# Kernel tuning notes

Measured on AMD Instinct MI355X. Metric: run time of the kernel, lower is better.

The kernel has to match this reference:

```python
import jax, jax.numpy as jnp
import numpy as np

NPOINT = 2048
NSAMPLE = 16
LEAKY = 0.1
BN_EPS = 1e-5


def square_distance(src, dst):
    # src [B,S,3], dst [B,N,3] -> [B,S,N] squared euclidean
    d = -2.0 * jnp.einsum('bsc,bnc->bsn', src, dst)
    d = d + jnp.sum(src * src, -1)[:, :, None]
    d = d + jnp.sum(dst * dst, -1)[:, None, :]
    return d


def furthest_point_sample(xyz, npoint):
    # xyz [B,N,3] -> idx [B,npoint]; matches pointnet2 CUDA (seed = index 0)
    B, N, _ = xyz.shape

    def step(carry, _):
        dist, far = carry  # dist [B,N], far [B]
        centroid = jnp.take_along_axis(xyz, far[:, None, None], axis=1)  # [B,1,3]
        d = jnp.sum((xyz - centroid) ** 2, axis=-1)
        dist = jnp.minimum(dist, d)
        nxt = jnp.argmax(dist, axis=-1).astype(jnp.int32)
        return (dist, nxt), far

    init = (jnp.full((B, N), 1e10, xyz.dtype), jnp.zeros((B,), jnp.int32))
    _, idxs = jax.lax.scan(step, init, None, length=npoint)
    return idxs.T  # [B, npoint]


def _gather_nbrs(p, i):
    # p [N,C], i [S,K] -> [S,K,C]
    return p[i]


gather_group = jax.vmap(_gather_nbrs)


def conv_bn_lrelu(x, W, g, b):
    # x [B,Cin,S,K], W [Cout,Cin]; 1x1 conv + train-mode BatchNorm2d + LeakyReLU
    y = jnp.einsum('oc,bcsk->bosk', W, x)
    mean = jnp.mean(y, axis=(0, 2, 3), keepdims=True)
    var = jnp.var(y, axis=(0, 2, 3), keepdims=True)
    y = (y - mean) * jax.lax.rsqrt(var + BN_EPS)
    y = y * g[None, :, None, None] + b[None, :, None, None]
    return jnp.where(y > 0, y, LEAKY * y)


def setup_inputs() -> dict:
    key = jax.random.key(0)
    ks = jax.random.split(key, 5)
    B, N, D = 4, 8192, 64
    return {
        'xyz': jax.random.normal(ks[0], (B, 3, N), jnp.float32),
        'points': jax.random.normal(ks[1], (B, D, N), jnp.float32),
        'conv0_w': jax.random.normal(ks[2], (64, 67), jnp.float32) * 0.05,
        'conv1_w': jax.random.normal(ks[3], (64, 64), jnp.float32) * 0.05,
        'conv2_w': jax.random.normal(ks[4], (128, 64), jnp.float32) * 0.05,
        'bn0_g': jnp.ones((64,), jnp.float32),
        'bn0_b': jnp.zeros((64,), jnp.float32),
        'bn1_g': jnp.ones((64,), jnp.float32),
        'bn1_b': jnp.zeros((64,), jnp.float32),
        'bn2_g': jnp.ones((128,), jnp.float32),
        'bn2_b': jnp.zeros((128,), jnp.float32),
    }


def reference(xyz, points, conv0_w, conv1_w, conv2_w,
              bn0_g, bn0_b, bn1_g, bn1_b, bn2_g, bn2_b):
    xyz_t = jnp.transpose(xyz, (0, 2, 1))      # [B,N,3]
    pts_t = jnp.transpose(points, (0, 2, 1))   # [B,N,D]

    fps_idx = furthest_point_sample(xyz_t, NPOINT)                       # [B,S]
    new_xyz = jnp.take_along_axis(xyz_t, fps_idx[:, :, None], axis=1)    # [B,S,3]

    sqrd = square_distance(new_xyz, xyz_t)                               # [B,S,N]
    _, idx = jax.lax.top_k(-sqrd, NSAMPLE)                               # [B,S,K]

    grouped_xyz = gather_group(xyz_t, idx)                               # [B,S,K,3]
    grouped_norm = grouped_xyz - new_xyz[:, :, None, :]
    grouped_pts = gather_group(pts_t, idx)                               # [B,S,K,D]
    new_points = jnp.concatenate([grouped_norm, grouped_pts], axis=-1)   # [B,S,K,D+3]
    new_points = jnp.transpose(new_points, (0, 3, 1, 2))                 # [B,D+3,S,K]

    for W, g, b in ((conv0_w, bn0_g, bn0_b), (conv1_w, bn1_g, bn1_b),
                    (conv2_w, bn2_g, bn2_b)):
        new_points = conv_bn_lrelu(new_points, W, g, b)

    feat = jnp.max(new_points, axis=-1)                                  # [B,128,S]
    return jnp.transpose(new_xyz, (0, 2, 1)), feat, fps_idx
```

## Files before the change

### kernel.cpp

```cpp
#include <hip/hip_runtime.h>
#include <hip/hip_bf16.h>

#define BB 4
#define NP 8192
#define SS 2048
#define KK 16
#define DD 64
#define NN (BB*SS*KK)
#define HEATERS 128

typedef float vf2 __attribute__((ext_vector_type(2)));

#if defined(__has_builtin)
#if __has_builtin(__builtin_amdgcn_permlane16_swap) && __has_builtin(__builtin_amdgcn_permlane32_swap)
#define HAVE_PERMLANE_SWAP 1
#endif
#endif

__device__ __forceinline__ float wave_max_f32(float v) {
  int x;
  x = __builtin_amdgcn_update_dpp(0, __float_as_int(v), 0xB1, 0xF, 0xF, true);
  v = fmaxf(v, __int_as_float(x));
  x = __builtin_amdgcn_update_dpp(0, __float_as_int(v), 0x4E, 0xF, 0xF, true);
  v = fmaxf(v, __int_as_float(x));
  x = __builtin_amdgcn_update_dpp(0, __float_as_int(v), 0x141, 0xF, 0xF, true);
  v = fmaxf(v, __int_as_float(x));
  x = __builtin_amdgcn_update_dpp(0, __float_as_int(v), 0x140, 0xF, 0xF, true);
  v = fmaxf(v, __int_as_float(x));
#ifdef HAVE_PERMLANE_SWAP
  {
    unsigned u = __float_as_uint(v);
    auto r16 = __builtin_amdgcn_permlane16_swap(u, u, false, false);
    v = fmaxf(__uint_as_float(r16[0]), __uint_as_float(r16[1]));
    unsigned u2 = __float_as_uint(v);
    auto r32 = __builtin_amdgcn_permlane32_swap(u2, u2, false, false);
    v = fmaxf(__uint_as_float(r32[0]), __uint_as_float(r32[1]));
  }
#else
  x = __builtin_amdgcn_ds_swizzle(__float_as_int(v), 0x401F);
  v = fmaxf(v, __int_as_float(x));
  v = fmaxf(v, __shfl_xor(v, 32, 64));
#endif
  return v;
}

__global__ __launch_bounds__(512) void fps_kernel(
    const float* __restrict__ xyz, float* __restrict__ newXyz,
    float* __restrict__ out, int* __restrict__ done)
{
  const int t = threadIdx.x;

  if (blockIdx.x >= BB) {
    float a0 = 1.0f, a1 = 1.1f, a2 = 1.2f, a3 = 1.3f;
    const float bm = 1.000001f, cm = 1e-7f;
    for (;;) {
      for (int k = 0; k < 1024; k++) {
        a0 = __builtin_fmaf(a0, bm, cm);
        a1 = __builtin_fmaf(a1, bm, cm);
        a2 = __builtin_fmaf(a2, bm, cm);
        a3 = __builtin_fmaf(a3, bm, cm);
      }
      if (__hip_atomic_load(done, __ATOMIC_RELAXED, __HIP_MEMORY_SCOPE_AGENT) >= BB)
        break;
    }
    if (a0 == 123.456f && a1 == 2.f && a2 == 3.f && a3 == 4.f)
      ((volatile int*)done)[1] = 1;
    return;
  }

  const int b = blockIdx.x;
  const float* xb = xyz + (size_t)b * 3 * NP;

  __shared__ float lx[NP], ly[NP], lz[NP];
  __shared__ int   wis[SS];
  __shared__ unsigned long long swin[3];

  vf2 px[8], py[8], pz[8], dist[8];
  const int i0 = t << 4;
#pragma unroll
  for (int h = 0; h < 8; h++) {
    int i = i0 + (h << 1);
    vf2 x = *(const vf2*)(xb + i);
    vf2 y = *(const vf2*)(xb + NP + i);
    vf2 z = *(const vf2*)(xb + 2 * NP + i);
    px[h] = x; py[h] = y; pz[h] = z;
    dist[h] = (vf2){1e10f, 1e10f};
    *(vf2*)(lx + i) = x; *(vf2*)(ly + i) = y; *(vf2*)(lz + i) = z;
  }
  if (t == 0) { wis[0] = 0; swin[0] = 0; swin[1] = 0; swin[2] = 0; }
  __syncthreads();

  float cx = lx[0], cy = ly[0], cz = lz[0];

  for (int it = 1; it < SS; ++it) {
    vf2 c2x = {cx, cx}, c2y = {cy, cy}, c2z = {cz, cz};
    vf2 lb = {-1.0f, -1.0f};
    {
#pragma clang fp contract(off)
#pragma unroll
      for (int h = 0; h < 8; h++) {
        vf2 dx = px[h] - c2x;
        vf2 dy = py[h] - c2y;
        vf2 dz = pz[h] - c2z;
        vf2 d  = (dx * dx + dy * dy) + dz * dz;
        vf2 dm = __builtin_elementwise_min(dist[h], d);
        dist[h] = dm;
        lb = __builtin_elementwise_max(lb, dm);
      }
    }
    float lbest = fmaxf(lb.x, lb.y);
    float Vw = wave_max_f32(lbest);
    int q = it % 3;
    if (lbest == Vw) {
      unsigned mi = 0u;
#pragma unroll
      for (int h = 7; h >= 0; h--) {
        unsigned base = (unsigned)(i0 + (h << 1));
        if (dist[h].y == Vw) mi = base + 1;
        if (dist[h].x == Vw) mi = base;
      }
      unsigned long long pk =
          ((unsigned long long)__float_as_uint(Vw) << 32) | (unsigned)(~mi);
      atomicMax(&swin[q], pk);
    }
    __syncthreads();
    unsigned long long pkf = swin[q];
    int ii = (int)(~((unsigned)pkf));
    if (t == 0) { wis[it] = ii; swin[(q + 2) % 3] = 0; }
    cx = lx[ii]; cy = ly[ii]; cz = lz[ii];
  }
  __syncthreads();

  float* outX = out;
  float* outI = out + 24576 + 1048576;
  for (int s = t; s < SS; s += 512) {
    int iw = wis[s];
    float x = lx[iw], y = ly[iw], z = lz[iw];
    size_t qq = (size_t)(b * SS + s);
    newXyz[qq * 3 + 0] = x;
    newXyz[qq * 3 + 1] = y;
    newXyz[qq * 3 + 2] = z;
    outX[(b * 3 + 0) * SS + s] = x;
    outX[(b * 3 + 1) * SS + s] = y;
    outX[(b * 3 + 2) * SS + s] = z;
    outI[b * SS + s] = (float)iw;
  }
  if (t == 0)
    __hip_atomic_fetch_add(done, 1, __ATOMIC_RELEASE, __HIP_MEMORY_SCOPE_AGENT);
}

__global__ __launch_bounds__(256) void knn_kernel(
    const float* __restrict__ xyz, const float* __restrict__ newXyz,
    int* __restrict__ knnIdx)
{
  const int t = threadIdx.x, w = t >> 6, l = t & 63;
  const int q = blockIdx.x * 4 + w;
  const int b = q >> 11;
  const float* xb = xyz + (size_t)b * 3 * NP;
  float qx = newXyz[q * 3], qy = newXyz[q * 3 + 1], qz = newXyz[q * 3 + 2];
  float ss = __fadd_rn(__fadd_rn(__fmul_rn(qx, qx), __fmul_rn(qy, qy)), __fmul_rn(qz, qz));
  float kd[16]; int ki[16];
#pragma unroll
  for (int j = 0; j < 16; j++) { kd[j] = __builtin_inff(); ki[j] = 0x7fffffff; }

  for (int m = 0; m < 128; m++) {
    int i = l + (m << 6);
    float x = xb[i], y = xb[NP + i], z = xb[2 * NP + i];
    float dot = __fadd_rn(__fadd_rn(__fmul_rn(x, qx), __fmul_rn(y, qy)), __fmul_rn(z, qz));
    float nn  = __fadd_rn(__fadd_rn(__fmul_rn(x, x), __fmul_rn(y, y)), __fmul_rn(z, z));
    float d   = __fadd_rn(__fadd_rn(__fmul_rn(-2.0f, dot), ss), nn);
    if (d < kd[15]) {
      kd[15] = d; ki[15] = i;
#pragma unroll
      for (int jj = 15; jj >= 1; jj--) {
        if (kd[jj] < kd[jj - 1]) {
          float td = kd[jj]; kd[jj] = kd[jj - 1]; kd[jj - 1] = td;
          int   ti = ki[jj]; ki[jj] = ki[jj - 1]; ki[jj - 1] = ti;
        }
      }
    }
  }

  __shared__ float sd[4 * 64 * 17];
  __shared__ int   sx[4 * 64 * 17];
  int base = (w * 64 + l) * 17;
#pragma unroll
  for (int j = 0; j < 16; j++) { sd[base + j] = kd[j]; sx[base + j] = ki[j]; }
  __syncthreads();

  int cur = 0; int outIdx = 0;
#pragma unroll 1
  for (int r = 0; r < 16; r++) {
    float hv = (cur < 16) ? sd[base + cur] : __builtin_inff();
    int   hi = (cur < 16) ? sx[base + cur] : 0x7fffffff;
    int   hl = l;
#pragma unroll
    for (int m2 = 1; m2 < 64; m2 <<= 1) {
      float ov = __shfl_xor(hv, m2, 64);
      int   oi = __shfl_xor(hi, m2, 64);
      int   ol = __shfl_xor(hl, m2, 64);
      if (ov < hv || (ov == hv && oi < hi)) { hv = ov; hi = oi; hl = ol; }
    }
    if (l == hl) cur++;
    if (l == r) outIdx = hi;
  }
  if (l < 16) knnIdx[q * 16 + l] = outIdx;
}

__global__ __launch_bounds__(256) void build_x0(
    const float* __restrict__ xyz, const float* __restrict__ points,
    const float* __restrict__ newXyz, const int* __restrict__ knnIdx,
    float* __restrict__ X)
{
  int n = blockIdx.x * 256 + threadIdx.x;
  int b = n >> 15;
  int q = n >> 4;
  int ip = knnIdx[n];
  const float* xb = xyz + (size_t)b * 3 * NP;
  X[(size_t)0 * NN + n] = xb[ip]          - newXyz[q * 3 + 0];
  X[(size_t)1 * NN + n] = xb[NP + ip]     - newXyz[q * 3 + 1];
  X[(size_t)2 * NN + n] = xb[2 * NP + ip] - newXyz[q * 3 + 2];
  const float* pb = points + (size_t)b * DD * NP;
#pragma unroll 8
  for (int d0 = 0; d0 < DD; d0++)
    X[(size_t)(3 + d0) * NN + n] = pb[(size_t)d0 * NP + ip];
}

template <int CIN, int COUT, bool BNIN>
__global__ __launch_bounds__(256) void conv_kernel(
    const float* __restrict__ X, const float* __restrict__ W,
    const float* __restrict__ ss, float* __restrict__ Y)
{
  __shared__ vf2 sss[CIN];
  if (BNIN) {
    for (int i = threadIdx.x; i < CIN; i += 256) sss[i] = ((const vf2*)ss)[i];
    __syncthreads();
  }
  int n = blockIdx.x * 256 + threadIdx.x;
  float x[CIN];
#pragma unroll
  for (int c = 0; c < CIN; c++) x[c] = X[(size_t)c * NN + n];
  if (BNIN) {
#pragma unroll
    for (int c = 0; c < CIN; c++) {
      vf2 p = sss[c];
      float v = fmaf(x[c], p.x, p.y);
      x[c] = v > 0.0f ? v : 0.1f * v;
    }
  }
#pragma unroll 1
  for (int o = 0; o < COUT; o += 4) {
    float a0 = 0.f, a1 = 0.f, a2 = 0.f, a3 = 0.f;
#pragma unroll
    for (int c = 0; c < CIN; c++) {
      float xv = x[c];
      a0 = fmaf(W[(o + 0) * CIN + c], xv, a0);
      a1 = fmaf(W[(o + 1) * CIN + c], xv, a1);
      a2 = fmaf(W[(o + 2) * CIN + c], xv, a2);
      a3 = fmaf(W[(o + 3) * CIN + c], xv, a3);
    }
    Y[(size_t)(o + 0) * NN + n] = a0;
    Y[(size_t)(o + 1) * NN + n] = a1;
    Y[(size_t)(o + 2) * NN + n] = a2;
    Y[(size_t)(o + 3) * NN + n] = a3;
  }
}

__global__ __launch_bounds__(256) void stats_kernel(
    const float* __restrict__ Y, float* __restrict__ stats)
{
  int c = blockIdx.y;
  int base = blockIdx.x * 4096 + threadIdx.x;
  const float* yc = Y + (size_t)c * NN;
  float s1 = 0.f, s2 = 0.f;
#pragma unroll
  for (int j = 0; j < 16; j++) {
    float v = yc[base + j * 256];
    s1 += v; s2 = fmaf(v, v, s2);
  }
#pragma unroll
  for (int m = 1; m < 64; m <<= 1) {
    s1 += __shfl_xor(s1, m, 64);
    s2 += __shfl_xor(s2, m, 64);
  }
  __shared__ float r1[4], r2[4];
  int w = threadIdx.x >> 6;
  if ((threadIdx.x & 63) == 0) { r1[w] = s1; r2[w] = s2; }
  __syncthreads();
  if (threadIdx.x == 0) {
    float t1 = r1[0] + r1[1] + r1[2] + r1[3];
    float t2 = r2[0] + r2[1] + r2[2] + r2[3];
    atomicAdd(&stats[c * 2], t1);
    atomicAdd(&stats[c * 2 + 1], t2);
  }
}

template <int C>
__global__ void finalize_kernel(const float* __restrict__ stats,
                                const float* __restrict__ g,
                                const float* __restrict__ bt,
                                float* __restrict__ ss)
{
  int c = threadIdx.x;
  if (c < C) {
    float mean = stats[c * 2] * (1.0f / NN);
    float var  = stats[c * 2 + 1] * (1.0f / NN) - mean * mean;
    float inv  = rsqrtf(var + 1e-5f);
    float sc = inv * g[c];
    float sh = bt[c] - mean * sc;
    ss[c * 2] = sc; ss[c * 2 + 1] = sh;
  }
}

__global__ __launch_bounds__(256) void maxk_kernel(
    const float* __restrict__ X, const float* __restrict__ ss,
    float* __restrict__ out)
{
  int m = blockIdx.x * 256 + threadIdx.x;
  int s = m & 2047;
  int o = (m >> 11) & 127;
  int b = m >> 18;
  float sc = ss[2 * o], sh = ss[2 * o + 1];
  const float4* p = (const float4*)(X + (size_t)o * NN + ((size_t)((b << 11) + s) << 4));
  float mx = -__builtin_inff();
#pragma unroll
  for (int j = 0; j < 4; j++) {
    float4 v4 = p[j];
    float a = fmaf(v4.x, sc, sh); a = a > 0.f ? a : 0.1f * a;
    float b2 = fmaf(v4.y, sc, sh); b2 = b2 > 0.f ? b2 : 0.1f * b2;
    float c = fmaf(v4.z, sc, sh); c = c > 0.f ? c : 0.1f * c;
    float d = fmaf(v4.w, sc, sh); d = d > 0.f ? d : 0.1f * d;
    mx = fmaxf(mx, fmaxf(fmaxf(a, b2), fmaxf(c, d)));
  }
  out[24576 + (size_t)((b << 7) + o) * SS + s] = mx;
}

extern "C" void kernel_launch(void* const* d_in, const int* in_sizes, int n_in,
                              void* d_out, int out_size, void* d_ws, size_t ws_size,
                              hipStream_t stream) {
  const float* xyz    = (const float*)d_in[0];
  const float* points = (const float*)d_in[1];
  const float* w0 = (const float*)d_in[2];
  const float* w1 = (const float*)d_in[3];
  const float* w2 = (const float*)d_in[4];
  const float* g0 = (const float*)d_in[5];
  const float* b0 = (const float*)d_in[6];
  const float* g1 = (const float*)d_in[7];
  const float* b1 = (const float*)d_in[8];
  const float* g2 = (const float*)d_in[9];
  const float* b2 = (const float*)d_in[10];
  float* out = (float*)d_out;

  float* wsf    = (float*)d_ws;
  float* newXyz = wsf;
  int*   knnIdx = (int*)(wsf + 24576);
  float* stats0 = wsf + 155648;
  float* stats1 = wsf + 155904;
  float* stats2 = wsf + 156160;
  float* ss0    = wsf + 156416;
  float* ss1    = wsf + 156672;
  float* ss2    = wsf + 156928;
  int*   done   = (int*)(wsf + 157440);
  float* Xa     = wsf + 160000;
  float* Xb     = wsf + 8941824;

  hipMemsetAsync(stats0, 0, 2048 * 4, stream);

  fps_kernel<<<BB + HEATERS, 512, 0, stream>>>(xyz, newXyz, out, done);
  knn_kernel<<<SS * BB / 4, 256, 0, stream>>>(xyz, newXyz, knnIdx);
  build_x0<<<NN / 256, 256, 0, stream>>>(xyz, points, newXyz, knnIdx, Xa);

  conv_kernel<67, 64, false><<<NN / 256, 256, 0, stream>>>(Xa, w0, nullptr, Xb);
  stats_kernel<<<dim3(32, 64), 256, 0, stream>>>(Xb, stats0);
  finalize_kernel<64><<<1, 128, 0, stream>>>(stats0, g0, b0, ss0);

  conv_kernel<64, 64, true><<<NN / 256, 256, 0, stream>>>(Xb, w1, ss0, Xa);
  stats_kernel<<<dim3(32, 64), 256, 0, stream>>>(Xa, stats1);
  finalize_kernel<64><<<1, 128, 0, stream>>>(stats1, g1, b1, ss1);

  conv_kernel<64, 128, true><<<NN / 256, 256, 0, stream>>>(Xa, w2, ss1, Xb);
  stats_kernel<<<dim3(32, 128), 256, 0, stream>>>(Xb, stats2);
  finalize_kernel<128><<<1, 128, 0, stream>>>(stats2, g2, b2, ss2);

  maxk_kernel<<<(BB * 128 * SS) / 256, 256, 0, stream>>>(Xb, ss2, out);
}
```

Measured before the change: 2.332 ms.

## Fuse gather into first conv, fold BN finalize into consumers, vectorize kNN loads

The neighbor gather is fused into the first 1x1 conv, so the 67-channel grouped tensor is never written to or re-read from global memory. The three BN finalize kernels are removed and each consumer kernel (conv_bn, maxk) recomputes scale and shift from the raw stats. The kNN scan now loads four points per lane with float4, which reduces load instructions but changes the order in which candidates are inserted. These changes cut launches and global traffic, at the cost of more registers in conv0 and some redundant per-thread BN arithmetic in maxk.

New measurement: 2.285 ms. -2.0%, faster.

```diff
diff --git a/kernel.cpp b/kernel.cpp
--- a/kernel.cpp
+++ b/kernel.cpp
@@ -163,19 +163,27 @@
 #pragma unroll
   for (int j = 0; j < 16; j++) { kd[j] = __builtin_inff(); ki[j] = 0x7fffffff; }
 
-  for (int m = 0; m < 128; m++) {
-    int i = l + (m << 6);
-    float x = xb[i], y = xb[NP + i], z = xb[2 * NP + i];
-    float dot = __fadd_rn(__fadd_rn(__fmul_rn(x, qx), __fmul_rn(y, qy)), __fmul_rn(z, qz));
-    float nn  = __fadd_rn(__fadd_rn(__fmul_rn(x, x), __fmul_rn(y, y)), __fmul_rn(z, z));
-    float d   = __fadd_rn(__fadd_rn(__fmul_rn(-2.0f, dot), ss), nn);
-    if (d < kd[15]) {
-      kd[15] = d; ki[15] = i;
-#pragma unroll
-      for (int jj = 15; jj >= 1; jj--) {
-        if (kd[jj] < kd[jj - 1]) {
-          float td = kd[jj]; kd[jj] = kd[jj - 1]; kd[jj - 1] = td;
-          int   ti = ki[jj]; ki[jj] = ki[jj - 1]; ki[jj - 1] = ti;
+  for (int m = 0; m < 32; m++) {
+    int i = (m << 8) + (l << 2);
+    float4 xv = *(const float4*)(xb + i);
+    float4 yv = *(const float4*)(xb + NP + i);
+    float4 zv = *(const float4*)(xb + 2 * NP + i);
+#pragma unroll
+    for (int c = 0; c < 4; c++) {
+      float x = (c == 0) ? xv.x : (c == 1) ? xv.y : (c == 2) ? xv.z : xv.w;
+      float y = (c == 0) ? yv.x : (c == 1) ? yv.y : (c == 2) ? yv.z : yv.w;
+      float z = (c == 0) ? zv.x : (c == 1) ? zv.y : (c == 2) ? zv.z : zv.w;
+      float dot = __fadd_rn(__fadd_rn(__fmul_rn(x, qx), __fmul_rn(y, qy)), __fmul_rn(z, qz));
+      float nn  = __fadd_rn(__fadd_rn(__fmul_rn(x, x), __fmul_rn(y, y)), __fmul_rn(z, z));
+      float d   = __fadd_rn(__fadd_rn(__fmul_rn(-2.0f, dot), ss), nn);
+      if (d < kd[15]) {
+        kd[15] = d; ki[15] = i + c;
+#pragma unroll
+        for (int jj = 15; jj >= 1; jj--) {
+          if (kd[jj] < kd[jj - 1]) {
+            float td = kd[jj]; kd[jj] = kd[jj - 1]; kd[jj - 1] = td;
+            int   ti = ki[jj]; ki[jj] = ki[jj - 1]; ki[jj - 1] = ti;
+          }
         }
       }
     }
@@ -207,46 +215,68 @@
   if (l < 16) knnIdx[q * 16 + l] = outIdx;
 }
 
-__global__ __launch_bounds__(256) void build_x0(
+__global__ __launch_bounds__(256) void conv0_kernel(
     const float* __restrict__ xyz, const float* __restrict__ points,
     const float* __restrict__ newXyz, const int* __restrict__ knnIdx,
-    float* __restrict__ X)
+    const float* __restrict__ W, float* __restrict__ Y)
 {
   int n = blockIdx.x * 256 + threadIdx.x;
   int b = n >> 15;
   int q = n >> 4;
   int ip = knnIdx[n];
   const float* xb = xyz + (size_t)b * 3 * NP;
-  X[(size_t)0 * NN + n] = xb[ip]          - newXyz[q * 3 + 0];
-  X[(size_t)1 * NN + n] = xb[NP + ip]     - newXyz[q * 3 + 1];
-  X[(size_t)2 * NN + n] = xb[2 * NP + ip] - newXyz[q * 3 + 2];
-  const float* pb = points + (size_t)b * DD * NP;
+  float x[67];
+  x[0] = xb[ip]          - newXyz[q * 3 + 0];
+  x[1] = xb[NP + ip]     - newXyz[q * 3 + 1];
+  x[2] = xb[2 * NP + ip] - newXyz[q * 3 + 2];
+  const float* pb = points + (size_t)b * DD * NP + ip;
 #pragma unroll 8
   for (int d0 = 0; d0 < DD; d0++)
-    X[(size_t)(3 + d0) * NN + n] = pb[(size_t)d0 * NP + ip];
-}
-
-template <int CIN, int COUT, bool BNIN>
-__global__ __launch_bounds__(256) void conv_kernel(
+    x[3 + d0] = pb[(size_t)d0 * NP];
+#pragma unroll 1
+  for (int o = 0; o < 64; o += 4) {
+    float a0 = 0.f, a1 = 0.f, a2 = 0.f, a3 = 0.f;
+#pragma unroll
+    for (int c = 0; c < 67; c++) {
+      float xv = x[c];
+      a0 = fmaf(W[(o + 0) * 67 + c], xv, a0);
+      a1 = fmaf(W[(o + 1) * 67 + c], xv, a1);
+      a2 = fmaf(W[(o + 2) * 67 + c], xv, a2);
+      a3 = fmaf(W[(o + 3) * 67 + c], xv, a3);
+    }
+    Y[(size_t)(o + 0) * NN + n] = a0;
+    Y[(size_t)(o + 1) * NN + n] = a1;
+    Y[(size_t)(o + 2) * NN + n] = a2;
+    Y[(size_t)(o + 3) * NN + n] = a3;
+  }
+}
+
+template <int CIN, int COUT>
+__global__ __launch_bounds__(256) void conv_bn_kernel(
     const float* __restrict__ X, const float* __restrict__ W,
-    const float* __restrict__ ss, float* __restrict__ Y)
+    const float* __restrict__ stats, const float* __restrict__ g,
+    const float* __restrict__ bt, float* __restrict__ Y)
 {
   __shared__ vf2 sss[CIN];
-  if (BNIN) {
-    for (int i = threadIdx.x; i < CIN; i += 256) sss[i] = ((const vf2*)ss)[i];
-    __syncthreads();
-  }
+  if (threadIdx.x < CIN) {
+    int c = threadIdx.x;
+    float mean = stats[c * 2] * (1.0f / NN);
+    float var  = stats[c * 2 + 1] * (1.0f / NN) - mean * mean;
+    float inv  = rsqrtf(var + 1e-5f);
+    float sc = inv * g[c];
+    float sh = bt[c] - mean * sc;
+    sss[c] = (vf2){sc, sh};
+  }
+  __syncthreads();
   int n = blockIdx.x * 256 + threadIdx.x;
   float x[CIN];
 #pragma unroll
   for (int c = 0; c < CIN; c++) x[c] = X[(size_t)c * NN + n];
-  if (BNIN) {
-#pragma unroll
-    for (int c = 0; c < CIN; c++) {
-      vf2 p = sss[c];
-      float v = fmaf(x[c], p.x, p.y);
-      x[c] = v > 0.0f ? v : 0.1f * v;
-    }
+#pragma unroll
+  for (int c = 0; c < CIN; c++) {
+    vf2 p = sss[c];
+    float v = fmaf(x[c], p.x, p.y);
+    x[c] = v > 0.0f ? v : 0.1f * v;
   }
 #pragma unroll 1
   for (int o = 0; o < COUT; o += 4) {
@@ -295,32 +325,20 @@
   }
 }
 
-template <int C>
-__global__ void finalize_kernel(const float* __restrict__ stats,
-                                const float* __restrict__ g,
-                                const float* __restrict__ bt,
-                                float* __restrict__ ss)
-{
-  int c = threadIdx.x;
-  if (c < C) {
-    float mean = stats[c * 2] * (1.0f / NN);
-    float var  = stats[c * 2 + 1] * (1.0f / NN) - mean * mean;
-    float inv  = rsqrtf(var + 1e-5f);
-    float sc = inv * g[c];
-    float sh = bt[c] - mean * sc;
-    ss[c * 2] = sc; ss[c * 2 + 1] = sh;
-  }
-}
-
 __global__ __launch_bounds__(256) void maxk_kernel(
-    const float* __restrict__ X, const float* __restrict__ ss,
+    const float* __restrict__ X, const float* __restrict__ stats,
+    const float* __restrict__ g, const float* __restrict__ bt,
     float* __restrict__ out)
 {
   int m = blockIdx.x * 256 + threadIdx.x;
   int s = m & 2047;
   int o = (m >> 11) & 127;
   int b = m >> 18;
-  float sc = ss[2 * o], sh = ss[2 * o + 1];
+  float mean = stats[o * 2] * (1.0f / NN);
+  float var  = stats[o * 2 + 1] * (1.0f / NN) - mean * mean;
+  float inv  = rsqrtf(var + 1e-5f);
+  float sc = inv * g[o];
+  float sh = bt[o] - mean * sc;
   const float4* p = (const float4*)(X + (size_t)o * NN + ((size_t)((b << 11) + s) << 4));
   float mx = -__builtin_inff();
 #pragma unroll
@@ -357,9 +375,6 @@
   float* stats0 = wsf + 155648;
   float* stats1 = wsf + 155904;
   float* stats2 = wsf + 156160;
-  float* ss0    = wsf + 156416;
-  float* ss1    = wsf + 156672;
-  float* ss2    = wsf + 156928;
   int*   done   = (int*)(wsf + 157440);
   float* Xa     = wsf + 160000;
   float* Xb     = wsf + 8941824;
@@ -368,19 +383,15 @@
 
   fps_kernel<<<BB + HEATERS, 512, 0, stream>>>(xyz, newXyz, out, done);
   knn_kernel<<<SS * BB / 4, 256, 0, stream>>>(xyz, newXyz, knnIdx);
-  build_x0<<<NN / 256, 256, 0, stream>>>(xyz, points, newXyz, knnIdx, Xa);
-
-  conv_kernel<67, 64, false><<<NN / 256, 256, 0, stream>>>(Xa, w0, nullptr, Xb);
+
+  conv0_kernel<<<NN / 256, 256, 0, stream>>>(xyz, points, newXyz, knnIdx, w0, Xb);
   stats_kernel<<<dim3(32, 64), 256, 0, stream>>>(Xb, stats0);
-  finalize_kernel<64><<<1, 128, 0, stream>>>(stats0, g0, b0, ss0);
-
-  conv_kernel<64, 64, true><<<NN / 256, 256, 0, stream>>>(Xb, w1, ss0, Xa);
+
+  conv_bn_kernel<64, 64><<<NN / 256, 256, 0, stream>>>(Xb, w1, stats0, g0, b0, Xa);
   stats_kernel<<<dim3(32, 64), 256, 0, stream>>>(Xa, stats1);
-  finalize_kernel<64><<<1, 128, 0, stream>>>(stats1, g1, b1, ss1);
-
-  conv_kernel<64, 128, true><<<NN / 256, 256, 0, stream>>>(Xa, w2, ss1, Xb);
+
+  conv_bn_kernel<64, 128><<<NN / 256, 256, 0, stream>>>(Xa, w2, stats1, g1, b1, Xb);
   stats_kernel<<<dim3(32, 128), 256, 0, stream>>>(Xb, stats2);
-  finalize_kernel<128><<<1, 128, 0, stream>>>(stats2, g2, b2, ss2);
-
-  maxk_kernel<<<(BB * 128 * SS) / 256, 256, 0, stream>>>(Xb, ss2, out);
-}
+
+  maxk_kernel<<<(BB * 128 * SS) / 256, 256, 0, stream>>>(Xb, stats2, g2, b2, out);
+}
```
